# Optimization experiments

Hardware: AMD Instinct MI355X
Metric: run time of the kernel (lower is better)

## Reference

```python
import jax, jax.numpy as jnp
import numpy as np

N, E = 10000, 320000
IN, HID, HEADS, OUT = 1280, 128, 4, 500
NEG_SLOPE = 0.2
BN_EPS = 1e-5


def gat_layer(x, src, dst, W, a_src, a_dst, b, concat):
    """PyG-style GATConv (single weight matrix, additive attention, scatter-softmax)."""
    n = x.shape[0]
    H, C = a_src.shape
    xp = (x @ W).reshape(n, H, C)                      # [N,H,C]
    s = jnp.sum(xp * a_src, axis=-1)                   # [N,H] src attention logits
    d = jnp.sum(xp * a_dst, axis=-1)                   # [N,H] dst attention logits
    e = jax.nn.leaky_relu(s[src] + d[dst], NEG_SLOPE)  # [Etot,H]
    # scatter-softmax over edges sharing the same destination node
    m = jax.ops.segment_max(e, dst, num_segments=n)
    ex = jnp.exp(e - m[dst])
    z = jax.ops.segment_sum(ex, dst, num_segments=n)
    alpha = ex / z[dst]                                # [Etot,H]
    out = jax.ops.segment_sum(alpha[:, :, None] * xp[src], dst, num_segments=n)  # [N,H,C]
    out = out.reshape(n, H * C) if concat else out.mean(axis=1)
    return out + b


def batch_norm(x, gamma, beta):
    mu = x.mean(axis=0)
    var = x.var(axis=0)  # biased, matches torch BN training normalization
    return (x - mu) * jax.lax.rsqrt(var + BN_EPS) * gamma + beta


def setup_inputs() -> dict:
    key = jax.random.key(0)
    ks = jax.random.split(key, 20)
    rn = lambda k, shape, s=0.05: jax.random.normal(k, shape, jnp.float32) * s
    HC = HID * HEADS
    return {
        "x": jax.random.normal(ks[0], (N, IN), jnp.float32),
        "edge_index": jax.random.randint(ks[1], (2, E), 0, N, jnp.int64 if jax.config.jax_enable_x64 else jnp.int32),
        "W1": rn(ks[2], (IN, HC)), "a_src1": rn(ks[3], (HEADS, HID)), "a_dst1": rn(ks[4], (HEADS, HID)), "b1": jnp.zeros((HC,), jnp.float32),
        "g1": jnp.ones((HC,), jnp.float32), "be1": jnp.zeros((HC,), jnp.float32),
        "W2": rn(ks[5], (HC, HC)), "a_src2": rn(ks[6], (HEADS, HID)), "a_dst2": rn(ks[7], (HEADS, HID)), "b2": jnp.zeros((HC,), jnp.float32),
        "g2": jnp.ones((HC,), jnp.float32), "be2": jnp.zeros((HC,), jnp.float32),
        "W3": rn(ks[8], (HC, OUT)), "a_src3": rn(ks[9], (1, OUT)), "a_dst3": rn(ks[10], (1, OUT)), "b3": jnp.zeros((OUT,), jnp.float32),
    }


def reference(x, edge_index, W1, a_src1, a_dst1, b1, g1, be1,
              W2, a_src2, a_dst2, b2, g2, be2, W3, a_src3, a_dst3, b3):
    n = x.shape[0]
    loops = jnp.arange(n, dtype=edge_index.dtype)
    src = jnp.concatenate([edge_index[0], loops])  # PyG add_self_loops=True
    dst = jnp.concatenate([edge_index[1], loops])
    h = gat_layer(x, src, dst, W1, a_src1, a_dst1, b1, concat=True)
    h = jax.nn.elu(batch_norm(h, g1, be1))
    h = gat_layer(h, src, dst, W2, a_src2, a_dst2, b2, concat=True)
    h = jax.nn.elu(batch_norm(h, g2, be2))
    return gat_layer(h, src, dst, W3, a_src3, a_dst3, b3, concat=False)
```

## Files before the change

### kernel.cpp

```cpp
#include <hip/hip_runtime.h>
#include <hip/hip_bf16.h>

#define NNODES 10000
#define NEDGES 320000
#define INF_   1280
#define HID_   128
#define HEADS_ 4
#define OUTF_  500
#define HC_    512
#define NEG_SLOPE 0.2f
#define BN_EPS 1e-5f

typedef __attribute__((ext_vector_type(8))) short short8x;
typedef __attribute__((ext_vector_type(4))) float f32x4;
typedef unsigned short ushort_t;
typedef unsigned int uint_t;

__device__ __forceinline__ ushort_t f2bf(float f) {
    uint_t u = __float_as_uint(f);
    u = (u + 0x7fffu + ((u >> 16) & 1u)) >> 16;
    return (ushort_t)u;
}
__device__ __forceinline__ float bf_lo(uint_t p) { return __uint_as_float(p << 16); }
__device__ __forceinline__ float bf_hi(uint_t p) { return __uint_as_float(p & 0xffff0000u); }
__device__ __forceinline__ float lrelu(float x) { return (x >= 0.f) ? x : NEG_SLOPE * x; }
__device__ __forceinline__ uint_t pack_bf16_rn(float a, float b) {
    __hip_bfloat162 h = __float22bfloat162_rn(make_float2(a, b));
    return *(uint_t*)&h;
}

#define CVX (NNODES * INF_ / 4)
#define CN1 (HC_ * INF_)
#define CN2 (HC_ * HC_)
#define CN3 (HC_ * HC_)
#define CZC (NNODES / 4)
__global__ void convall_kernel(const float* __restrict__ x,
                               const float* __restrict__ W1,
                               const float* __restrict__ W2,
                               const float* __restrict__ W3,
                               ushort_t* __restrict__ x_bf,
                               ushort_t* __restrict__ Wt1,
                               ushort_t* __restrict__ Wt2,
                               ushort_t* __restrict__ Wt3,
                               uint4* __restrict__ zc) {
    int i = blockIdx.x * blockDim.x + threadIdx.x;
    if (i < CVX) {
        float4 v = ((const float4*)x)[i];
        ((uint2*)x_bf)[i] = make_uint2(pack_bf16_rn(v.x, v.y), pack_bf16_rn(v.z, v.w));
    } else if (i < CVX + CN1) {
        int j = i - CVX;
        int n = j / INF_, k = j - n * INF_;
        Wt1[j] = f2bf(W1[(size_t)k * HC_ + n]);
    } else if (i < CVX + CN1 + CN2) {
        int j = i - CVX - CN1;
        int n = j / HC_, k = j - n * HC_;
        Wt2[j] = f2bf(W2[(size_t)k * HC_ + n]);
    } else if (i < CVX + CN1 + CN2 + CN3) {
        int j = i - CVX - CN1 - CN2;
        int n = j / HC_, k = j - n * HC_;
        Wt3[j] = (n < OUTF_) ? f2bf(W3[(size_t)k * OUTF_ + n]) : (ushort_t)0;
    } else if (i < CVX + CN1 + CN2 + CN3 + CZC) {
        zc[i - CVX - CN1 - CN2 - CN3] = make_uint4(0, 0, 0, 0);
    }
}

__global__ void count_kernel(const int* __restrict__ dst, int* __restrict__ counts, int E) {
    int e = blockIdx.x * blockDim.x + threadIdx.x;
    if (e < E) atomicAdd(&counts[dst[e]], 1);
}

__global__ __launch_bounds__(1024) void scan_fused_kernel(const int* __restrict__ counts,
                                                          int* __restrict__ offsets,
                                                          int* __restrict__ cursor, int n) {
    __shared__ int tsum[1024];
    int t = threadIdx.x;
    int base = t * 10;
    int v[10];
    int s = 0;
#pragma unroll
    for (int k = 0; k < 10; ++k) {
        int i = base + k;
        int c = (i < n) ? counts[i] : 0;
        v[k] = s;
        s += c;
    }
    tsum[t] = s;
    __syncthreads();
    for (int off = 1; off < 1024; off <<= 1) {
        int u = (t >= off) ? tsum[t - off] : 0;
        __syncthreads();
        tsum[t] += u;
        __syncthreads();
    }
    int prefix = (t > 0) ? tsum[t - 1] : 0;
#pragma unroll
    for (int k = 0; k < 10; ++k) {
        int i = base + k;
        if (i < n) {
            int o = prefix + v[k];
            offsets[i] = o;
            cursor[i] = o;
        }
    }
    if (t == 1023) offsets[n] = tsum[1023];
}

__global__ void scatter_kernel(const int* __restrict__ src, const int* __restrict__ dst,
                               int* __restrict__ cursor, int* __restrict__ esrc, int E) {
    int e = blockIdx.x * blockDim.x + threadIdx.x;
    if (e < E) {
        int p = atomicAdd(&cursor[dst[e]], 1);
        esrc[p] = src[e];
    }
}

#define LDT 40

__global__ __launch_bounds__(256) void gemm_kernel(
    const ushort_t* __restrict__ A,
    const ushort_t* __restrict__ Bt,
    ushort_t* __restrict__ Cb,
    int M, int K)
{
    __shared__ __align__(16) ushort_t As[64 * LDT];
    __shared__ __align__(16) ushort_t Bs[128 * LDT];

    int m0 = blockIdx.y * 64;
    int n0 = blockIdx.x * 128;

    int tid  = threadIdx.x;
    int lane = tid & 63;
    int w    = tid >> 6;
    int wm   = (w & 1) * 32;
    int wn   = (w >> 1) * 64;
    int quad = lane >> 4;
    int c16  = lane & 15;

    f32x4 acc[2][4];
#pragma unroll
    for (int i = 0; i < 2; ++i)
#pragma unroll
        for (int j = 0; j < 4; ++j)
#pragma unroll
            for (int r = 0; r < 4; ++r) acc[i][j][r] = 0.0f;

    int sr = tid >> 2;
    int sk = (tid & 3) * 8;
    int gm = m0 + sr;  if (gm > M - 1) gm = M - 1;
    const ushort_t* aptr = A + (size_t)gm * K + sk;
    int br0 = tid >> 2;
    int bk0 = (tid & 3) * 8;
    int br1 = (256 + tid) >> 2;
    int bk1 = bk0;
    const ushort_t* bptr0 = Bt + (size_t)(n0 + br0) * K + bk0;
    const ushort_t* bptr1 = Bt + (size_t)(n0 + br1) * K + bk1;

    uint4 av  = *(const uint4*)(aptr);
    uint4 bv0 = *(const uint4*)(bptr0);
    uint4 bv1 = *(const uint4*)(bptr1);

    for (int k0 = 0; k0 < K; k0 += 32) {
        *(uint4*)&As[sr * LDT + sk]   = av;
        *(uint4*)&Bs[br0 * LDT + bk0] = bv0;
        *(uint4*)&Bs[br1 * LDT + bk1] = bv1;
        __syncthreads();

        short8x af0 = *(const short8x*)&As[(wm +      c16) * LDT + quad * 8];
        short8x af1 = *(const short8x*)&As[(wm + 16 + c16) * LDT + quad * 8];
        short8x bf[4];
#pragma unroll
        for (int nt = 0; nt < 4; ++nt)
            bf[nt] = *(const short8x*)&Bs[(wn + nt * 16 + c16) * LDT + quad * 8];

        if (k0 + 32 < K) {
            av  = *(const uint4*)(aptr  + k0 + 32);
            bv0 = *(const uint4*)(bptr0 + k0 + 32);
            bv1 = *(const uint4*)(bptr1 + k0 + 32);
        }

#pragma unroll
        for (int nt = 0; nt < 4; ++nt) {
            acc[0][nt] = __builtin_amdgcn_mfma_f32_16x16x32_bf16(af0, bf[nt], acc[0][nt], 0, 0, 0);
            acc[1][nt] = __builtin_amdgcn_mfma_f32_16x16x32_bf16(af1, bf[nt], acc[1][nt], 0, 0, 0);
        }
        __syncthreads();
    }

#pragma unroll
    for (int mt = 0; mt < 2; ++mt) {
#pragma unroll
        for (int r = 0; r < 4; ++r) {
            int row = m0 + wm + mt * 16 + quad * 4 + r;
            if (row < M) {
#pragma unroll
                for (int nt = 0; nt < 4; ++nt) {
                    int col = n0 + wn + nt * 16 + c16;
                    Cb[(size_t)row * 512 + col] = f2bf(acc[mt][nt][r]);
                }
            }
        }
    }
}

template<int H>
__global__ __launch_bounds__(256) void logits_kernel(
    const uint4* __restrict__ xpb4,
    const float* __restrict__ aS, const float* __restrict__ aD,
    float* __restrict__ s_log, float* __restrict__ d_log, int OUTC)
{
    int node = blockIdx.x * 4 + (threadIdx.x >> 6);
    if (node >= NNODES) return;
    int lane = threadIdx.x & 63;
    uint4 p = xpb4[(size_t)node * 64 + lane];
    float xv[8] = {bf_lo(p.x), bf_hi(p.x), bf_lo(p.y), bf_hi(p.y),
                   bf_lo(p.z), bf_hi(p.z), bf_lo(p.w), bf_hi(p.w)};
    int cbase = lane * 8;
    float sv = 0.f, dv = 0.f;
    if (cbase + 7 < OUTC) {
        float4 a0 = ((const float4*)aS)[lane * 2];
        float4 a1 = ((const float4*)aS)[lane * 2 + 1];
        float4 b0 = ((const float4*)aD)[lane * 2];
        float4 b1 = ((const float4*)aD)[lane * 2 + 1];
        sv = xv[0]*a0.x + xv[1]*a0.y + xv[2]*a0.z + xv[3]*a0.w
           + xv[4]*a1.x + xv[5]*a1.y + xv[6]*a1.z + xv[7]*a1.w;
        dv = xv[0]*b0.x + xv[1]*b0.y + xv[2]*b0.z + xv[3]*b0.w
           + xv[4]*b1.x + xv[5]*b1.y + xv[6]*b1.z + xv[7]*b1.w;
    } else {
#pragma unroll
        for (int k = 0; k < 8; ++k) {
            int c = cbase + k;
            if (c < OUTC) { sv += xv[k] * aS[c]; dv += xv[k] * aD[c]; }
        }
    }
    int grp = (H == 4) ? 16 : 64;
    for (int off = 1; off < grp; off <<= 1) {
        sv += __shfl_xor(sv, off);
        dv += __shfl_xor(dv, off);
    }
    if ((lane & (grp - 1)) == 0) {
        int h = (H == 4) ? (lane >> 4) : 0;
        s_log[node * H + h] = sv;
        d_log[node * H + h] = dv;
    }
}

__device__ __forceinline__ void acc8(float* acc, uint4 q, float w) {
    acc[0] += w * bf_lo(q.x); acc[1] += w * bf_hi(q.x);
    acc[2] += w * bf_lo(q.y); acc[3] += w * bf_hi(q.y);
    acc[4] += w * bf_lo(q.z); acc[5] += w * bf_hi(q.z);
    acc[6] += w * bf_lo(q.w); acc[7] += w * bf_hi(q.w);
}

template<int H>
__global__ __launch_bounds__(256) void gather_fused_kernel(
    const uint4* __restrict__ xpb4,
    const int* __restrict__ offsets, const int* __restrict__ esrc,
    const float* __restrict__ s_log,
    const float* __restrict__ d_log,
    const float* __restrict__ bias,
    float* __restrict__ out,
    int OUTC, int ldo)
{
    int id = blockIdx.x;
    int xcd = id & 7;
    int slice = xcd >> 1;
    int sub2 = xcd & 1;
    int wv = threadIdx.x >> 6;
    int node = (id >> 3) * 8 + sub2 * 4 + wv;
    if (node >= NNODES) return;
    int lane = threadIdx.x & 63;
    int esub = lane >> 4;
    int l16 = lane & 15;
    int h = (H == 4) ? slice : 0;
    int rowoff = slice * 16 + l16;

    float dh = d_log[node * H + h];
    float c0 = lrelu(s_log[node * H + h] + dh);

    float acc[8];
    float z;
    if (esub == 0) {
        uint4 p = xpb4[(size_t)node * 64 + rowoff];
        acc[0] = bf_lo(p.x); acc[1] = bf_hi(p.x);
        acc[2] = bf_lo(p.y); acc[3] = bf_hi(p.y);
        acc[4] = bf_lo(p.z); acc[5] = bf_hi(p.z);
        acc[6] = bf_lo(p.w); acc[7] = bf_hi(p.w);
        z = 1.0f;
    } else {
#pragma unroll
        for (int k = 0; k < 8; ++k) acc[k] = 0.f;
        z = 0.f;
    }

    int e0 = offsets[node], e1 = offsets[node + 1];
    int j = e0 + esub;
    for (; j + 12 < e1; j += 16) {
        int s0 = esrc[j], s1 = esrc[j + 4], s2 = esrc[j + 8], s3 = esrc[j + 12];
        uint4 q0 = xpb4[(size_t)s0 * 64 + rowoff];
        uint4 q1 = xpb4[(size_t)s1 * 64 + rowoff];
        uint4 q2 = xpb4[(size_t)s2 * 64 + rowoff];
        uint4 q3 = xpb4[(size_t)s3 * 64 + rowoff];
        float w0 = __expf(lrelu(s_log[s0 * H + h] + dh) - c0);
        float w1 = __expf(lrelu(s_log[s1 * H + h] + dh) - c0);
        float w2 = __expf(lrelu(s_log[s2 * H + h] + dh) - c0);
        float w3 = __expf(lrelu(s_log[s3 * H + h] + dh) - c0);
        acc8(acc, q0, w0);
        acc8(acc, q1, w1);
        acc8(acc, q2, w2);
        acc8(acc, q3, w3);
        z += w0 + w1 + w2 + w3;
    }
    for (; j < e1; j += 4) {
        int s0 = esrc[j];
        uint4 q0 = xpb4[(size_t)s0 * 64 + rowoff];
        float w0 = __expf(lrelu(s_log[s0 * H + h] + dh) - c0);
        acc8(acc, q0, w0);
        z += w0;
    }

#pragma unroll
    for (int k = 0; k < 8; ++k) {
        acc[k] += __shfl_xor(acc[k], 16);
        acc[k] += __shfl_xor(acc[k], 32);
    }
    z += __shfl_xor(z, 16);
    z += __shfl_xor(z, 32);

    if (esub == 0) {
        float zi = 1.0f / z;
        int cbase = slice * 128 + l16 * 8;
        size_t ob = (size_t)node * ldo + cbase;
        if (cbase + 7 < OUTC) {
            float4 o0 = make_float4(acc[0] * zi + bias[cbase + 0], acc[1] * zi + bias[cbase + 1],
                                    acc[2] * zi + bias[cbase + 2], acc[3] * zi + bias[cbase + 3]);
            float4 o1 = make_float4(acc[4] * zi + bias[cbase + 4], acc[5] * zi + bias[cbase + 5],
                                    acc[6] * zi + bias[cbase + 6], acc[7] * zi + bias[cbase + 7]);
            *(float4*)(out + ob) = o0;
            *(float4*)(out + ob + 4) = o1;
        } else {
#pragma unroll
            for (int k = 0; k < 8; ++k) {
                int c = cbase + k;
                if (c < OUTC) out[ob + k] = acc[k] * zi + bias[c];
            }
        }
    }
}

__global__ __launch_bounds__(512) void bn_stats_kernel(const float* __restrict__ h,
                                                       float* __restrict__ psum,
                                                       float* __restrict__ psumsq) {
    int c = threadIdx.x;
    int b = blockIdx.x;
    float sm = 0.f, sq = 0.f;
    for (int r = b; r < NNODES; r += 64) {
        float v = h[(size_t)r * 512 + c];
        sm += v;
        sq += v * v;
    }
    psum[b * 512 + c] = sm;
    psumsq[b * 512 + c] = sq;
}

__global__ __launch_bounds__(256) void bn_apply_kernel(const float* __restrict__ h,
                                                       const float* __restrict__ psum,
                                                       const float* __restrict__ psumsq,
                                                       const float* __restrict__ gamma,
                                                       const float* __restrict__ beta,
                                                       uint_t* __restrict__ hbf) {
    int t = threadIdx.x, b = blockIdx.x;
    int c0 = t * 2, c1 = c0 + 1;
    float sm0 = 0.f, sq0 = 0.f, sm1 = 0.f, sq1 = 0.f;
    for (int k = 0; k < 64; ++k) {
        sm0 += psum[k * 512 + c0];   sq0 += psumsq[k * 512 + c0];
        sm1 += psum[k * 512 + c1];   sq1 += psumsq[k * 512 + c1];
    }
    const float invN = 1.0f / (float)NNODES;
    float mu0 = sm0 * invN, mu1 = sm1 * invN;
    float var0 = sq0 * invN - mu0 * mu0;
    float var1 = sq1 * invN - mu1 * mu1;
    float sc0 = gamma[c0] * rsqrtf(var0 + BN_EPS);
    float sc1 = gamma[c1] * rsqrtf(var1 + BN_EPS);
    float sh0 = beta[c0] - mu0 * sc0;
    float sh1 = beta[c1] - mu1 * sc1;
    for (int r = b; r < NNODES; r += 256) {
        float2 hv = ((const float2*)(h + (size_t)r * 512))[t];
        float v0 = hv.x * sc0 + sh0;
        float v1 = hv.y * sc1 + sh1;
        v0 = (v0 > 0.f) ? v0 : (__expf(v0) - 1.0f);
        v1 = (v1 > 0.f) ? v1 : (__expf(v1) - 1.0f);
        hbf[r * 256 + t] = ((uint_t)f2bf(v1) << 16) | (uint_t)f2bf(v0);
    }
}

extern "C" void kernel_launch(void* const* d_in, const int* in_sizes, int n_in,
                              void* d_out, int out_size, void* d_ws, size_t ws_size,
                              hipStream_t stream) {
    const float* x      = (const float*)d_in[0];
    const int*   ei     = (const int*)d_in[1];
    const float* W1     = (const float*)d_in[2];
    const float* a_src1 = (const float*)d_in[3];
    const float* a_dst1 = (const float*)d_in[4];
    const float* b1     = (const float*)d_in[5];
    const float* g1     = (const float*)d_in[6];
    const float* be1    = (const float*)d_in[7];
    const float* W2     = (const float*)d_in[8];
    const float* a_src2 = (const float*)d_in[9];
    const float* a_dst2 = (const float*)d_in[10];
    const float* b2     = (const float*)d_in[11];
    const float* g2     = (const float*)d_in[12];
    const float* be2    = (const float*)d_in[13];
    const float* W3     = (const float*)d_in[14];
    const float* a_src3 = (const float*)d_in[15];
    const float* a_dst3 = (const float*)d_in[16];
    const float* b3     = (const float*)d_in[17];
    float* out = (float*)d_out;

    const int* e_src = ei;
    const int* e_dst = ei + NEDGES;

    char* w = (char*)d_ws;
    ushort_t* x_bf = (ushort_t*)w;
    float*    hbuf = (float*)w;
    w += (size_t)NNODES * INF_ * sizeof(ushort_t);
    uint_t* xpb = (uint_t*)w;  w += (size_t)NNODES * HC_ * sizeof(ushort_t);
    uint_t* hbf = (uint_t*)w;  w += (size_t)NNODES * HC_ * sizeof(ushort_t);
    ushort_t* Wt1 = (ushort_t*)w; w += (size_t)HC_ * INF_ * sizeof(ushort_t);
    ushort_t* Wt2 = (ushort_t*)w; w += (size_t)HC_ * HC_ * sizeof(ushort_t);
    ushort_t* Wt3 = (ushort_t*)w; w += (size_t)HC_ * HC_ * sizeof(ushort_t);
    int* counts  = (int*)w;    w += NNODES * sizeof(int);
    float* s_log = (float*)w;  w += NNODES * HEADS_ * sizeof(float);
    float* d_log = (float*)w;  w += NNODES * HEADS_ * sizeof(float);
    float* psum  = (float*)w;  w += 64 * HC_ * sizeof(float);
    float* psumsq= (float*)w;  w += 64 * HC_ * sizeof(float);
    int* offsets = (int*)w;    w += (NNODES + 1) * sizeof(int);
    int* cursor  = (int*)w;    w += NNODES * sizeof(int);
    int* esrc    = (int*)w;    w += NEDGES * sizeof(int);

    dim3 gg(HC_ / 128, (NNODES + 63) / 64);
    const int lgGrid = (NNODES + 3) / 4;
    const int gaGrid = ((NNODES + 7) / 8) * 8;

    {
        int TOT = CVX + CN1 + CN2 + CN3 + CZC;
        convall_kernel<<<(TOT + 255) / 256, 256, 0, stream>>>(x, W1, W2, W3,
            x_bf, Wt1, Wt2, Wt3, (uint4*)counts);
    }
    count_kernel<<<(NEDGES + 255) / 256, 256, 0, stream>>>(e_dst, counts, NEDGES);
    scan_fused_kernel<<<1, 1024, 0, stream>>>(counts, offsets, cursor, NNODES);
    scatter_kernel<<<(NEDGES + 255) / 256, 256, 0, stream>>>(e_src, e_dst, cursor, esrc, NEDGES);

    gemm_kernel<<<gg, 256, 0, stream>>>(x_bf, Wt1, (ushort_t*)xpb, NNODES, INF_);
    logits_kernel<HEADS_><<<lgGrid, 256, 0, stream>>>((const uint4*)xpb, a_src1, a_dst1, s_log, d_log, HC_);
    gather_fused_kernel<HEADS_><<<gaGrid, 256, 0, stream>>>((const uint4*)xpb, offsets, esrc,
        s_log, d_log, b1, hbuf, HC_, HC_);
    bn_stats_kernel<<<64, 512, 0, stream>>>(hbuf, psum, psumsq);
    bn_apply_kernel<<<256, 256, 0, stream>>>(hbuf, psum, psumsq, g1, be1, hbf);

    gemm_kernel<<<gg, 256, 0, stream>>>((const ushort_t*)hbf, Wt2, (ushort_t*)xpb, NNODES, HC_);
    logits_kernel<HEADS_><<<lgGrid, 256, 0, stream>>>((const uint4*)xpb, a_src2, a_dst2, s_log, d_log, HC_);
    gather_fused_kernel<HEADS_><<<gaGrid, 256, 0, stream>>>((const uint4*)xpb, offsets, esrc,
        s_log, d_log, b2, hbuf, HC_, HC_);
    bn_stats_kernel<<<64, 512, 0, stream>>>(hbuf, psum, psumsq);
    bn_apply_kernel<<<256, 256, 0, stream>>>(hbuf, psum, psumsq, g2, be2, hbf);

    gemm_kernel<<<gg, 256, 0, stream>>>((const ushort_t*)hbf, Wt3, (ushort_t*)xpb, NNODES, HC_);
    logits_kernel<1><<<lgGrid, 256, 0, stream>>>((const uint4*)xpb, a_src3, a_dst3, s_log, d_log, OUTF_);
    gather_fused_kernel<1><<<gaGrid, 256, 0, stream>>>((const uint4*)xpb, offsets, esrc,
        s_log, d_log, b3, out, OUTF_, OUTF_);
}
```

Baseline: 470.6 us.

## Fuse attention-logit computation into GEMM epilogue and use wave-shuffle scan

Computes the per-node source and destination attention logits inside the GEMM epilogue from fp32 accumulators. This removes the three separate logits kernels and their re-read of the bf16 projection. For the single-head third layer, partial logits from each column tile are combined with atomicAdd, so bn_apply now zeroes the logit buffers first. The single-block prefix scan also replaces its 10-step shared-memory Hillis-Steele loop with wave shuffles plus a small cross-wave scan, cutting barriers. Logits now come from unrounded fp32 values rather than bf16, which slightly changes numerics, and the layer-3 float atomics make summation order nondeterministic.

```diff
diff --git a/kernel.cpp b/kernel.cpp
--- a/kernel.cpp
+++ b/kernel.cpp
@@ -72,8 +72,9 @@
 __global__ __launch_bounds__(1024) void scan_fused_kernel(const int* __restrict__ counts,
                                                           int* __restrict__ offsets,
                                                           int* __restrict__ cursor, int n) {
-    __shared__ int tsum[1024];
+    __shared__ int wsum[16];
     int t = threadIdx.x;
+    int lane = t & 63, wv = t >> 6;
     int base = t * 10;
     int v[10];
     int s = 0;
@@ -84,25 +85,36 @@
         v[k] = s;
         s += c;
     }
-    tsum[t] = s;
+    int incl = s;
+#pragma unroll
+    for (int off = 1; off < 64; off <<= 1) {
+        int u = __shfl_up(incl, off, 64);
+        if (lane >= off) incl += u;
+    }
+    if (lane == 63) wsum[wv] = incl;
     __syncthreads();
-    for (int off = 1; off < 1024; off <<= 1) {
-        int u = (t >= off) ? tsum[t - off] : 0;
-        __syncthreads();
-        tsum[t] += u;
-        __syncthreads();
-    }
-    int prefix = (t > 0) ? tsum[t - 1] : 0;
+    if (t < 16) {
+        int ws = wsum[t];
+        int in2 = ws;
+#pragma unroll
+        for (int off = 1; off < 16; off <<= 1) {
+            int u = __shfl_up(in2, off, 64);
+            if (t >= off) in2 += u;
+        }
+        wsum[t] = in2 - ws;
+    }
+    __syncthreads();
+    int basep = wsum[wv] + (incl - s);
 #pragma unroll
     for (int k = 0; k < 10; ++k) {
         int i = base + k;
         if (i < n) {
-            int o = prefix + v[k];
+            int o = basep + v[k];
             offsets[i] = o;
             cursor[i] = o;
         }
     }
-    if (t == 1023) offsets[n] = tsum[1023];
+    if (t == 1023) offsets[n] = basep + s;
 }
 
 __global__ void scatter_kernel(const int* __restrict__ src, const int* __restrict__ dst,
@@ -116,14 +128,20 @@
 
 #define LDT 40
 
+template<int LOGIT>
 __global__ __launch_bounds__(256) void gemm_kernel(
     const ushort_t* __restrict__ A,
     const ushort_t* __restrict__ Bt,
     ushort_t* __restrict__ Cb,
+    const float* __restrict__ aS,
+    const float* __restrict__ aD,
+    float* __restrict__ s_log,
+    float* __restrict__ d_log,
     int M, int K)
 {
     __shared__ __align__(16) ushort_t As[64 * LDT];
     __shared__ __align__(16) ushort_t Bs[128 * LDT];
+    __shared__ float sred[64][2], dred[64][2];
 
     int m0 = blockIdx.y * 64;
     int n0 = blockIdx.x * 128;
@@ -200,47 +218,54 @@
             }
         }
     }
-}
-
-template<int H>
-__global__ __launch_bounds__(256) void logits_kernel(
-    const uint4* __restrict__ xpb4,
-    const float* __restrict__ aS, const float* __restrict__ aD,
-    float* __restrict__ s_log, float* __restrict__ d_log, int OUTC)
-{
-    int node = blockIdx.x * 4 + (threadIdx.x >> 6);
-    if (node >= NNODES) return;
-    int lane = threadIdx.x & 63;
-    uint4 p = xpb4[(size_t)node * 64 + lane];
-    float xv[8] = {bf_lo(p.x), bf_hi(p.x), bf_lo(p.y), bf_hi(p.y),
-                   bf_lo(p.z), bf_hi(p.z), bf_lo(p.w), bf_hi(p.w)};
-    int cbase = lane * 8;
-    float sv = 0.f, dv = 0.f;
-    if (cbase + 7 < OUTC) {
-        float4 a0 = ((const float4*)aS)[lane * 2];
-        float4 a1 = ((const float4*)aS)[lane * 2 + 1];
-        float4 b0 = ((const float4*)aD)[lane * 2];
-        float4 b1 = ((const float4*)aD)[lane * 2 + 1];
-        sv = xv[0]*a0.x + xv[1]*a0.y + xv[2]*a0.z + xv[3]*a0.w
-           + xv[4]*a1.x + xv[5]*a1.y + xv[6]*a1.z + xv[7]*a1.w;
-        dv = xv[0]*b0.x + xv[1]*b0.y + xv[2]*b0.z + xv[3]*b0.w
-           + xv[4]*b1.x + xv[5]*b1.y + xv[6]*b1.z + xv[7]*b1.w;
-    } else {
-#pragma unroll
-        for (int k = 0; k < 8; ++k) {
-            int c = cbase + k;
-            if (c < OUTC) { sv += xv[k] * aS[c]; dv += xv[k] * aD[c]; }
-        }
-    }
-    int grp = (H == 4) ? 16 : 64;
-    for (int off = 1; off < grp; off <<= 1) {
-        sv += __shfl_xor(sv, off);
-        dv += __shfl_xor(dv, off);
-    }
-    if ((lane & (grp - 1)) == 0) {
-        int h = (H == 4) ? (lane >> 4) : 0;
-        s_log[node * H + h] = sv;
-        d_log[node * H + h] = dv;
+
+    float as_[4], ad_[4];
+#pragma unroll
+    for (int nt = 0; nt < 4; ++nt) {
+        int colg = n0 + wn + nt * 16 + c16;
+        if (LOGIT == 4) {
+            as_[nt] = aS[colg];
+            ad_[nt] = aD[colg];
+        } else {
+            as_[nt] = (colg < OUTF_) ? aS[colg] : 0.f;
+            ad_[nt] = (colg < OUTF_) ? aD[colg] : 0.f;
+        }
+    }
+#pragma unroll
+    for (int mt = 0; mt < 2; ++mt) {
+#pragma unroll
+        for (int r = 0; r < 4; ++r) {
+            float ps = acc[mt][0][r] * as_[0] + acc[mt][1][r] * as_[1]
+                     + acc[mt][2][r] * as_[2] + acc[mt][3][r] * as_[3];
+            float pd = acc[mt][0][r] * ad_[0] + acc[mt][1][r] * ad_[1]
+                     + acc[mt][2][r] * ad_[2] + acc[mt][3][r] * ad_[3];
+#pragma unroll
+            for (int off = 1; off < 16; off <<= 1) {
+                ps += __shfl_xor(ps, off);
+                pd += __shfl_xor(pd, off);
+            }
+            if (c16 == 0) {
+                int rl = wm + mt * 16 + quad * 4 + r;
+                sred[rl][wn >> 6] = ps;
+                dred[rl][wn >> 6] = pd;
+            }
+        }
+    }
+    __syncthreads();
+    if (tid < 64) {
+        int row = m0 + tid;
+        if (row < M) {
+            float s = sred[tid][0] + sred[tid][1];
+            float d = dred[tid][0] + dred[tid][1];
+            if (LOGIT == 4) {
+                int h = n0 >> 7;
+                s_log[row * 4 + h] = s;
+                d_log[row * 4 + h] = d;
+            } else {
+                atomicAdd(&s_log[row], s);
+                atomicAdd(&d_log[row], d);
+            }
+        }
     }
 }
 
@@ -367,8 +392,14 @@
                                                        const float* __restrict__ psumsq,
                                                        const float* __restrict__ gamma,
                                                        const float* __restrict__ beta,
-                                                       uint_t* __restrict__ hbf) {
+                                                       uint_t* __restrict__ hbf,
+                                                       float* __restrict__ zs,
+                                                       float* __restrict__ zd) {
     int t = threadIdx.x, b = blockIdx.x;
+    if (zs) {
+        int gid = b * 256 + t;
+        if (gid < NNODES) { zs[gid] = 0.f; zd[gid] = 0.f; }
+    }
     int c0 = t * 2, c1 = c0 + 1;
     float sm0 = 0.f, sq0 = 0.f, sm1 = 0.f, sq1 = 0.f;
     for (int k = 0; k < 64; ++k) {
@@ -438,7 +469,6 @@
     int* esrc    = (int*)w;    w += NEDGES * sizeof(int);
 
     dim3 gg(HC_ / 128, (NNODES + 63) / 64);
-    const int lgGrid = (NNODES + 3) / 4;
     const int gaGrid = ((NNODES + 7) / 8) * 8;
 
     {
@@ -450,22 +480,22 @@
     scan_fused_kernel<<<1, 1024, 0, stream>>>(counts, offsets, cursor, NNODES);
     scatter_kernel<<<(NEDGES + 255) / 256, 256, 0, stream>>>(e_src, e_dst, cursor, esrc, NEDGES);
 
-    gemm_kernel<<<gg, 256, 0, stream>>>(x_bf, Wt1, (ushort_t*)xpb, NNODES, INF_);
-    logits_kernel<HEADS_><<<lgGrid, 256, 0, stream>>>((const uint4*)xpb, a_src1, a_dst1, s_log, d_log, HC_);
+    gemm_kernel<4><<<gg, 256, 0, stream>>>(x_bf, Wt1, (ushort_t*)xpb,
+        a_src1, a_dst1, s_log, d_log, NNODES, INF_);
     gather_fused_kernel<HEADS_><<<gaGrid, 256, 0, stream>>>((const uint4*)xpb, offsets, esrc,
         s_log, d_log, b1, hbuf, HC_, HC_);
     bn_stats_kernel<<<64, 512, 0, stream>>>(hbuf, psum, psumsq);
-    bn_apply_kernel<<<256, 256, 0, stream>>>(hbuf, psum, psumsq, g1, be1, hbf);
-
-    gemm_kernel<<<gg, 256, 0, stream>>>((const ushort_t*)hbf, Wt2, (ushort_t*)xpb, NNODES, HC_);
-    logits_kernel<HEADS_><<<lgGrid, 256, 0, stream>>>((const uint4*)xpb, a_src2, a_dst2, s_log, d_log, HC_);
+    bn_apply_kernel<<<256, 256, 0, stream>>>(hbuf, psum, psumsq, g1, be1, hbf, nullptr, nullptr);
+
+    gemm_kernel<4><<<gg, 256, 0, stream>>>((const ushort_t*)hbf, Wt2, (ushort_t*)xpb,
+        a_src2, a_dst2, s_log, d_log, NNODES, HC_);
     gather_fused_kernel<HEADS_><<<gaGrid, 256, 0, stream>>>((const uint4*)xpb, offsets, esrc,
         s_log, d_log, b2, hbuf, HC_, HC_);
     bn_stats_kernel<<<64, 512, 0, stream>>>(hbuf, psum, psumsq);
-    bn_apply_kernel<<<256, 256, 0, stream>>>(hbuf, psum, psumsq, g2, be2, hbf);
-
-    gemm_kernel<<<gg, 256, 0, stream>>>((const ushort_t*)hbf, Wt3, (ushort_t*)xpb, NNODES, HC_);
-    logits_kernel<1><<<lgGrid, 256, 0, stream>>>((const uint4*)xpb, a_src3, a_dst3, s_log, d_log, OUTF_);
+    bn_apply_kernel<<<256, 256, 0, stream>>>(hbuf, psum, psumsq, g2, be2, hbf, s_log, d_log);
+
+    gemm_kernel<1><<<gg, 256, 0, stream>>>((const ushort_t*)hbf, Wt3, (ushort_t*)xpb,
+        a_src3, a_dst3, s_log, d_log, NNODES, HC_);
     gather_fused_kernel<1><<<gaGrid, 256, 0, stream>>>((const uint4*)xpb, offsets, esrc,
         s_log, d_log, b3, out, OUTF_, OUTF_);
 }
```

New measurement: 461.8 us. Within noise of the previous version (-1.9%).
